# Performance work log

Measured on AMD Instinct MI355X. Metric: run time of the kernel, lower is better.

## Reference

```python
import jax, jax.numpy as jnp
import numpy as np

RADIUS2 = 0.03 ** 2
SIM_THRESH = 0.7
EPS = 1e-8


def setup_inputs() -> dict:
    key = jax.random.key(0)
    k1, k2, k3, k4, k5, k6, k7 = jax.random.split(key, 7)
    B, N, D = 2, 6144, 32
    # points in a 0.3-side cube so radius 0.03 gives realistic neighbor counts
    points = jax.random.uniform(k1, (B, N, 3), dtype=jnp.float32) * 0.3
    embeddings = jax.random.normal(k2, (B, N, D), dtype=jnp.float32)
    leaf_mask = jax.random.randint(k3, (B, N), 0, 2, dtype=jnp.int32)
    # consistency_net: Linear(2D, D) -> ReLU -> Linear(D, D)
    W1 = jax.random.normal(k4, (2 * D, D), dtype=jnp.float32) * (1.0 / np.sqrt(2 * D))
    b1 = jax.random.normal(k5, (D,), dtype=jnp.float32) * 0.01
    W2 = jax.random.normal(k6, (D, D), dtype=jnp.float32) * (1.0 / np.sqrt(D))
    b2 = jax.random.normal(k7, (D,), dtype=jnp.float32) * 0.01
    return {"points": points, "embeddings": embeddings, "leaf_mask": leaf_mask,
            "W1": W1, "b1": b1, "W2": W2, "b2": b2}


def reference(points, embeddings, leaf_mask, W1, b1, W2, b2):
    # points: [B,N,3], embeddings: [B,N,D], leaf_mask: [B,N] int (0/1)
    dt = embeddings.dtype
    leaf = leaf_mask > 0  # [B,N] bool

    # pairwise squared distances via the Gram trick (avoids [B,N,N,3])
    pn = jnp.sum(points * points, axis=-1)                      # [B,N]
    gram = jnp.einsum('bic,bjc->bij', points, points)           # [B,N,N]
    d2 = jnp.maximum(pn[:, :, None] + pn[:, None, :] - 2.0 * gram, 0.0)

    # neighbor mask: within radius AND neighbor is leaf (matches dist<0.03 & leaf_mask)
    nb = (d2 < RADIUS2) & leaf[:, None, :]                      # [B,N,N]

    # cosine similarity with torch's eps clamp on norms
    enorm = jnp.maximum(jnp.linalg.norm(embeddings, axis=-1), EPS)  # [B,N]
    inner = jnp.einsum('bid,bjd->bij', embeddings, embeddings)      # [B,N,N]
    sims = inner / (enorm[:, :, None] * enorm[:, None, :])

    sim_mask = nb & (sims > SIM_THRESH)                          # [B,N,N]
    cnt_nb = jnp.sum(nb, axis=-1)                                # [B,N]
    cnt_sim = jnp.sum(sim_mask, axis=-1)                         # [B,N]

    # mean of similar-neighbor embeddings
    sum_sim = jnp.einsum('bij,bjd->bid', sim_mask.astype(dt), embeddings)
    mean_sim = sum_sim / jnp.maximum(cnt_sim, 1).astype(dt)[..., None]

    # consistency MLP on [center_embedding, mean_similar]
    combined = jnp.concatenate([embeddings, mean_sim], axis=-1)  # [B,N,2D]
    h = jax.nn.relu(jnp.einsum('bnk,kd->bnd', combined, W1) + b1)
    out = jnp.einsum('bnk,kd->bnd', h, W2) + b2                  # [B,N,D]

    # refine only leaf points with >1 neighbor and >0 similar neighbors
    cond = leaf & (cnt_nb > 1) & (cnt_sim > 0)                   # [B,N]
    refined = jnp.where(cond[..., None], out, embeddings)

    # per-batch early exit: sum(leaf_mask) < 10 -> unchanged
    batch_ok = jnp.sum(leaf_mask, axis=-1) >= 10                 # [B]
    return jnp.where(batch_ok[:, None, None], refined, embeddings)
```

## Files before the change

### kernel.cpp

```cpp
#include <hip/hip_runtime.h>

#define NPTS    6144
#define DIM     32
#define NB      2
#define NCELL   1000
#define R2      0.0009f
#define NWAVES  4
#define BLOCK   (NWAVES * 64)
#define LEAFBIT 8192
#define PPT     6
#define NBCAP   128

__device__ __forceinline__ int cellof(float x) {
    int c = (int)(x * (10.0f / 0.3f));
    return min(max(c, 0), 9);
}

#define WS_LEAF   0
#define WS_CSTART 4
#define WS_SORTED 2008

__global__ __launch_bounds__(1024)
void build_cells(const float* __restrict__ points, const int* __restrict__ leaf,
                 int* __restrict__ ws)
{
    __shared__ int s_hist[1024];
    __shared__ int s_cursor[1024];
    __shared__ int s_wsum[16];
    __shared__ int s_leaf;

    const int t = threadIdx.x;
    const int b = blockIdx.x;
    const int w = t >> 6, lane = t & 63;

    s_hist[t] = 0;
    if (t == 0) s_leaf = 0;

    float px[PPT], py[PPT], pz[PPT];
    int   pc[PPT], pw[PPT];

    __syncthreads();

    int lc = 0;
    #pragma unroll
    for (int r = 0; r < PPT; ++r) {
        const int i  = r * 1024 + t;
        const int gi = b * NPTS + i;
        px[r] = points[gi * 3 + 0];
        py[r] = points[gi * 3 + 1];
        pz[r] = points[gi * 3 + 2];
        const int lf = leaf[gi] > 0 ? 1 : 0;
        lc += lf;
        pc[r] = (cellof(pz[r]) * 10 + cellof(py[r])) * 10 + cellof(px[r]);
        pw[r] = i + (lf ? LEAFBIT : 0);
        atomicAdd(&s_hist[pc[r]], 1);
    }
    #pragma unroll
    for (int off = 32; off > 0; off >>= 1) lc += __shfl_down(lc, off);
    if (lane == 0) atomicAdd(&s_leaf, lc);
    __syncthreads();

    const int v = s_hist[t];
    int x = v;
    #pragma unroll
    for (int off = 1; off < 64; off <<= 1) {
        const int y = __shfl_up(x, off);
        if (lane >= off) x += y;
    }
    if (lane == 63) s_wsum[w] = x;
    __syncthreads();
    if (t < 16) {
        int wv = s_wsum[t];
        #pragma unroll
        for (int off = 1; off < 16; off <<= 1) {
            const int y = __shfl_up(wv, off);
            if (t >= off) wv += y;
        }
        s_wsum[t] = wv;
    }
    __syncthreads();
    const int incl = x + (w > 0 ? s_wsum[w - 1] : 0);
    s_cursor[t] = incl - v;

    if (t < NCELL) ws[WS_CSTART + b * (NCELL + 1) + t + 1] = incl;
    if (t == 0) {
        ws[WS_CSTART + b * (NCELL + 1)] = 0;
        ws[WS_LEAF + b] = s_leaf;
    }
    __syncthreads();

    float4* sorted = (float4*)(ws + WS_SORTED) + (size_t)b * NPTS;
    #pragma unroll
    for (int r = 0; r < PPT; ++r) {
        const int pos = atomicAdd(&s_cursor[pc[r]], 1);
        sorted[pos] = make_float4(px[r], py[r], pz[r], (float)pw[r]);
    }
}

__global__ __launch_bounds__(BLOCK)
void refine(const float* __restrict__ emb,
            const float* __restrict__ W1, const float* __restrict__ b1,
            const float* __restrict__ W2, const float* __restrict__ b2,
            const int* __restrict__ ws, float* __restrict__ out)
{
    __shared__ __align__(16) float s_ei[NWAVES][DIM];
    __shared__ float s_mean[NWAVES][DIM];
    __shared__ float s_h[NWAVES][DIM];
    __shared__ int   s_nb[NWAVES][NBCAP];
    __shared__ int   s_sv[NWAVES][NBCAP];

    const int tid  = threadIdx.x;
    const int wid  = tid >> 6;
    const int lane = tid & 63;
    const int s    = blockIdx.x * NWAVES + wid;
    const int b    = s / NPTS;
    const int slot = s - b * NPTS;

    const float4* srt  = (const float4*)(ws + WS_SORTED) + (size_t)b * NPTS;
    const int*    cst  = ws + WS_CSTART + b * (NCELL + 1);
    const float*  embB = emb + (size_t)b * NPTS * DIM;

    const float4 P  = srt[slot];
    const int    iw = (int)P.w;
    const int    io = iw & (LEAFBIT - 1);
    const bool   li = (iw & LEAFBIT) != 0;
    const bool   ok = ws[WS_LEAF + b] >= 10;

    const float4* e4   = (const float4*)(embB + (size_t)io * DIM);
    float4*       out4 = (float4*)(out + ((size_t)b * NPTS + io) * DIM);

    if (!(ok && li)) {
        if (lane < DIM / 4) out4[lane] = e4[lane];
        return;
    }

    if (lane < DIM) s_ei[wid][lane] = ((const float*)e4)[lane];

    float ni2 = 0.0f;
    #pragma unroll
    for (int d = 0; d < DIM; ++d) { const float v = s_ei[wid][d]; ni2 += v * v; }
    const float rni = 1.0f / fmaxf(sqrtf(ni2), 1e-8f);

    const int cx = cellof(P.x), cy = cellof(P.y), cz = cellof(P.z);

    int begv = 0, lenv = 0;
    if (lane < 9) {
        const int z = cz + lane / 3 - 1;
        const int y = cy + lane % 3 - 1;
        if ((unsigned)z <= 9u && (unsigned)y <= 9u) {
            const int rowb = (z * 10 + y) * 10;
            const int c0   = rowb + max(cx - 1, 0);
            const int c1   = rowb + min(cx + 1, 9);
            begv = cst[c0];
            lenv = cst[c1 + 1] - begv;
        }
    }
    const int rb0 = __shfl(begv, 0), rb1 = __shfl(begv, 1), rb2 = __shfl(begv, 2);
    const int rb3 = __shfl(begv, 3), rb4 = __shfl(begv, 4), rb5 = __shfl(begv, 5);
    const int rb6 = __shfl(begv, 6), rb7 = __shfl(begv, 7), rb8 = __shfl(begv, 8);
    const int ln0 = __shfl(lenv, 0), ln1 = __shfl(lenv, 1), ln2 = __shfl(lenv, 2);
    const int ln3 = __shfl(lenv, 3), ln4 = __shfl(lenv, 4), ln5 = __shfl(lenv, 5);
    const int ln6 = __shfl(lenv, 6), ln7 = __shfl(lenv, 7), ln8 = __shfl(lenv, 8);
    const int pf1 = ln0,       pf2 = pf1 + ln1, pf3 = pf2 + ln2;
    const int pf4 = pf3 + ln3, pf5 = pf4 + ln4, pf6 = pf5 + ln5;
    const int pf7 = pf6 + ln6, pf8 = pf7 + ln7, pf9 = pf8 + ln8;

    int nbcnt = 0;
    for (int base = 0; base < pf9; base += 64) {
        const int g = base + lane;
        int j = 0;
        if (g < pf9) j = rb8 + g - pf8;
        if (g < pf8) j = rb7 + g - pf7;
        if (g < pf7) j = rb6 + g - pf6;
        if (g < pf6) j = rb5 + g - pf5;
        if (g < pf5) j = rb4 + g - pf4;
        if (g < pf4) j = rb3 + g - pf3;
        if (g < pf3) j = rb2 + g - pf2;
        if (g < pf2) j = rb1 + g - pf1;
        if (g < pf1) j = rb0 + g;
        const float4 Q  = srt[j];
        const float dx = Q.x - P.x, dy = Q.y - P.y, dz = Q.z - P.z;
        const float d2 = dx * dx + dy * dy + dz * dz;
        const int   jw = (int)Q.w;
        const bool  nb = (g < pf9) && (d2 < R2) && ((jw & LEAFBIT) != 0);
        const unsigned long long m = __ballot(nb);
        if (nb) {
            const int pos = nbcnt + __popcll(m & ((1ull << lane) - 1ull));
            if (pos < NBCAP) s_nb[wid][pos] = jw & (LEAFBIT - 1);
        }
        nbcnt += __popcll(m);
    }
    const int cnt_nb = nbcnt;

    int csim = 0;
    const int nh = min(cnt_nb, NBCAP);
    for (int h0 = 0; h0 < nh; h0 += 64) {
        const int h = h0 + lane;
        bool surv = false;
        int  jo   = 0;
        if (h < nh) {
            jo = s_nb[wid][h];
            const float4* ej4 = (const float4*)(embB + (size_t)jo * DIM);
            float dot = 0.0f, nj2 = 0.0f;
            #pragma unroll
            for (int k = 0; k < DIM / 4; ++k) {
                const float4 v = ej4[k];
                const float4 a = *(const float4*)&s_ei[wid][4 * k];
                dot += a.x * v.x + a.y * v.y + a.z * v.z + a.w * v.w;
                nj2 += v.x * v.x + v.y * v.y + v.z * v.z + v.w * v.w;
            }
            const float rnj = 1.0f / fmaxf(sqrtf(nj2), 1e-8f);
            surv = (dot * rni * rnj) > 0.7f;
        }
        const unsigned long long m = __ballot(surv);
        if (surv) {
            const int pos = csim + __popcll(m & ((1ull << lane) - 1ull));
            s_sv[wid][pos] = jo;
        }
        csim += __popcll(m);
    }

    const bool cond = (cnt_nb > 1) && (csim > 0);

    if (lane < DIM) {
        if (!cond) {
            out[((size_t)b * NPTS + io) * DIM + lane] = s_ei[wid][lane];
        } else {
            float msum = 0.0f;
            for (int v = 0; v < csim; ++v)
                msum += embB[(size_t)s_sv[wid][v] * DIM + lane];
            s_mean[wid][lane] = msum / (float)csim;

            float a0 = b1[lane], a1 = 0.0f;
            #pragma unroll
            for (int k = 0; k < DIM; k += 2) {
                a0 = fmaf(s_ei[wid][k],     W1[k * DIM + lane],       a0);
                a1 = fmaf(s_ei[wid][k + 1], W1[(k + 1) * DIM + lane], a1);
            }
            #pragma unroll
            for (int k = 0; k < DIM; k += 2) {
                a0 = fmaf(s_mean[wid][k],     W1[(DIM + k) * DIM + lane],     a0);
                a1 = fmaf(s_mean[wid][k + 1], W1[(DIM + k + 1) * DIM + lane], a1);
            }
            s_h[wid][lane] = fmaxf(a0 + a1, 0.0f);
            float c0 = b2[lane], c1 = 0.0f;
            #pragma unroll
            for (int k = 0; k < DIM; k += 2) {
                c0 = fmaf(s_h[wid][k],     W2[k * DIM + lane],       c0);
                c1 = fmaf(s_h[wid][k + 1], W2[(k + 1) * DIM + lane], c1);
            }
            out[((size_t)b * NPTS + io) * DIM + lane] = c0 + c1;
        }
    }
}

extern "C" void kernel_launch(void* const* d_in, const int* in_sizes, int n_in,
                              void* d_out, int out_size, void* d_ws, size_t ws_size,
                              hipStream_t stream) {
    const float* points = (const float*)d_in[0];
    const float* emb    = (const float*)d_in[1];
    const int*   leaf   = (const int*)d_in[2];
    const float* W1     = (const float*)d_in[3];
    const float* b1     = (const float*)d_in[4];
    const float* W2     = (const float*)d_in[5];
    const float* b2     = (const float*)d_in[6];
    float*       outp   = (float*)d_out;
    int*         ws     = (int*)d_ws;

    build_cells<<<NB, 1024, 0, stream>>>(points, leaf, ws);

    const int grid = (NB * NPTS) / NWAVES;
    refine<<<grid, BLOCK, 0, stream>>>(emb, W1, b1, W2, b2, ws, outp);
}
```

Measured before the change: 86.00 us.

## Overlap passthrough copy with cell build and split per-neighbor work across half-waves

Extra blocks in the cell-build launch now copy the whole embedding tensor to the output, so refine only writes points that actually get refined and returns early for everything else. Refine computes the centre norm with a shuffle reduction, and the similarity, mean and MLP stages split the 32-dim work across both wave halves, combining them with a cross-half shuffle. This removes idle lanes and the per-point copy path from refine. In exchange the output is written twice for refined points, and correctness depends on the copy kernel finishing before refine, which stream order guarantees.

```diff
diff --git a/kernel.cpp b/kernel.cpp
--- a/kernel.cpp
+++ b/kernel.cpp
@@ -10,6 +10,7 @@
 #define LEAFBIT 8192
 #define PPT     6
 #define NBCAP   128
+#define COPYBLK 64
 
 __device__ __forceinline__ int cellof(float x) {
     int c = (int)(x * (10.0f / 0.3f));
@@ -22,12 +23,23 @@
 
 __global__ __launch_bounds__(1024)
 void build_cells(const float* __restrict__ points, const int* __restrict__ leaf,
+                 const float* __restrict__ emb, float* __restrict__ out,
                  int* __restrict__ ws)
 {
     __shared__ int s_hist[1024];
     __shared__ int s_cursor[1024];
     __shared__ int s_wsum[16];
     __shared__ int s_leaf;
+
+    if (blockIdx.x >= NB) {
+        const int cb = blockIdx.x - NB;
+        const float4* src = (const float4*)emb;
+        float4*       dst = (float4*)out;
+        const int total = NB * NPTS * (DIM / 4);
+        for (int i = cb * 1024 + threadIdx.x; i < total; i += COPYBLK * 1024)
+            dst[i] = src[i];
+        return;
+    }
 
     const int t = threadIdx.x;
     const int b = blockIdx.x;
@@ -116,29 +128,24 @@
     const int b    = s / NPTS;
     const int slot = s - b * NPTS;
 
+    if (ws[WS_LEAF + b] < 10) return;
+
     const float4* srt  = (const float4*)(ws + WS_SORTED) + (size_t)b * NPTS;
     const int*    cst  = ws + WS_CSTART + b * (NCELL + 1);
     const float*  embB = emb + (size_t)b * NPTS * DIM;
 
     const float4 P  = srt[slot];
     const int    iw = (int)P.w;
-    const int    io = iw & (LEAFBIT - 1);
-    const bool   li = (iw & LEAFBIT) != 0;
-    const bool   ok = ws[WS_LEAF + b] >= 10;
-
-    const float4* e4   = (const float4*)(embB + (size_t)io * DIM);
-    float4*       out4 = (float4*)(out + ((size_t)b * NPTS + io) * DIM);
-
-    if (!(ok && li)) {
-        if (lane < DIM / 4) out4[lane] = e4[lane];
-        return;
-    }
-
-    if (lane < DIM) s_ei[wid][lane] = ((const float*)e4)[lane];
-
-    float ni2 = 0.0f;
-    #pragma unroll
-    for (int d = 0; d < DIM; ++d) { const float v = s_ei[wid][d]; ni2 += v * v; }
+    if (!(iw & LEAFBIT)) return;
+    const int io = iw & (LEAFBIT - 1);
+
+    const float* ei = embB + (size_t)io * DIM;
+    float ev = 0.0f;
+    if (lane < DIM) { ev = ei[lane]; s_ei[wid][lane] = ev; }
+    float nsq = ev * ev;
+    #pragma unroll
+    for (int off = 16; off > 0; off >>= 1) nsq += __shfl_xor(nsq, off);
+    const float ni2 = __shfl(nsq, 0);
     const float rni = 1.0f / fmaxf(sqrtf(ni2), 1e-8f);
 
     const int cx = cellof(P.x), cy = cellof(P.y), cz = cellof(P.z);
@@ -192,23 +199,29 @@
     }
     const int cnt_nb = nbcnt;
 
+    const int d    = lane & 31;
+    const int half = lane >> 5;
     int csim = 0;
     const int nh = min(cnt_nb, NBCAP);
-    for (int h0 = 0; h0 < nh; h0 += 64) {
-        const int h = h0 + lane;
-        bool surv = false;
-        int  jo   = 0;
+    for (int h0 = 0; h0 < nh; h0 += 32) {
+        const int h = h0 + d;
+        float dot = 0.0f, nj2 = 0.0f;
+        int   jo  = 0;
         if (h < nh) {
             jo = s_nb[wid][h];
-            const float4* ej4 = (const float4*)(embB + (size_t)jo * DIM);
-            float dot = 0.0f, nj2 = 0.0f;
+            const float4* ej4 = (const float4*)(embB + (size_t)jo * DIM) + half * 4;
             #pragma unroll
-            for (int k = 0; k < DIM / 4; ++k) {
+            for (int k = 0; k < 4; ++k) {
                 const float4 v = ej4[k];
-                const float4 a = *(const float4*)&s_ei[wid][4 * k];
+                const float4 a = *(const float4*)&s_ei[wid][16 * half + 4 * k];
                 dot += a.x * v.x + a.y * v.y + a.z * v.z + a.w * v.w;
                 nj2 += v.x * v.x + v.y * v.y + v.z * v.z + v.w * v.w;
             }
+        }
+        dot += __shfl_xor(dot, 32);
+        nj2 += __shfl_xor(nj2, 32);
+        bool surv = false;
+        if (h < nh && half == 0) {
             const float rnj = 1.0f / fmaxf(sqrtf(nj2), 1e-8f);
             surv = (dot * rni * rnj) > 0.7f;
         }
@@ -220,38 +233,37 @@
         csim += __popcll(m);
     }
 
-    const bool cond = (cnt_nb > 1) && (csim > 0);
-
-    if (lane < DIM) {
-        if (!cond) {
-            out[((size_t)b * NPTS + io) * DIM + lane] = s_ei[wid][lane];
-        } else {
-            float msum = 0.0f;
-            for (int v = 0; v < csim; ++v)
-                msum += embB[(size_t)s_sv[wid][v] * DIM + lane];
-            s_mean[wid][lane] = msum / (float)csim;
-
-            float a0 = b1[lane], a1 = 0.0f;
-            #pragma unroll
-            for (int k = 0; k < DIM; k += 2) {
-                a0 = fmaf(s_ei[wid][k],     W1[k * DIM + lane],       a0);
-                a1 = fmaf(s_ei[wid][k + 1], W1[(k + 1) * DIM + lane], a1);
-            }
-            #pragma unroll
-            for (int k = 0; k < DIM; k += 2) {
-                a0 = fmaf(s_mean[wid][k],     W1[(DIM + k) * DIM + lane],     a0);
-                a1 = fmaf(s_mean[wid][k + 1], W1[(DIM + k + 1) * DIM + lane], a1);
-            }
-            s_h[wid][lane] = fmaxf(a0 + a1, 0.0f);
-            float c0 = b2[lane], c1 = 0.0f;
-            #pragma unroll
-            for (int k = 0; k < DIM; k += 2) {
-                c0 = fmaf(s_h[wid][k],     W2[k * DIM + lane],       c0);
-                c1 = fmaf(s_h[wid][k + 1], W2[(k + 1) * DIM + lane], c1);
-            }
-            out[((size_t)b * NPTS + io) * DIM + lane] = c0 + c1;
-        }
-    }
+    if (!((cnt_nb > 1) && (csim > 0))) return;
+
+    float msum = 0.0f;
+    for (int v = half; v < csim; v += 2)
+        msum += embB[(size_t)s_sv[wid][v] * DIM + d];
+    msum += __shfl_xor(msum, 32);
+    if (half == 0) s_mean[wid][d] = msum / (float)csim;
+
+    float a = (half == 0) ? b1[d] : 0.0f;
+    #pragma unroll
+    for (int k = 0; k < 16; ++k) {
+        const int kk = half * 16 + k;
+        a = fmaf(s_ei[wid][kk], W1[kk * DIM + d], a);
+    }
+    #pragma unroll
+    for (int k = 0; k < 16; ++k) {
+        const int kk = half * 16 + k;
+        a = fmaf(s_mean[wid][kk], W1[(DIM + kk) * DIM + d], a);
+    }
+    a += __shfl_xor(a, 32);
+    if (half == 0) s_h[wid][d] = fmaxf(a, 0.0f);
+
+    float c = (half == 0) ? b2[d] : 0.0f;
+    #pragma unroll
+    for (int k = 0; k < 16; ++k) {
+        const int kk = half * 16 + k;
+        c = fmaf(s_h[wid][kk], W2[kk * DIM + d], c);
+    }
+    c += __shfl_xor(c, 32);
+    if (half == 0)
+        out[((size_t)b * NPTS + io) * DIM + d] = c;
 }
 
 extern "C" void kernel_launch(void* const* d_in, const int* in_sizes, int n_in,
@@ -267,7 +279,7 @@
     float*       outp   = (float*)d_out;
     int*         ws     = (int*)d_ws;
 
-    build_cells<<<NB, 1024, 0, stream>>>(points, leaf, ws);
+    build_cells<<<NB + COPYBLK, 1024, 0, stream>>>(points, leaf, emb, outp, ws);
 
     const int grid = (NB * NPTS) / NWAVES;
     refine<<<grid, BLOCK, 0, stream>>>(emb, W1, b1, W2, b2, ws, outp);
```

Result: no change. 86.85 us (+1.0%).
